# Optimization experiments

Hardware: AMD Instinct MI355X
Metric: run time of the kernel (lower is better)

Reference implementation:

```python
import jax, jax.numpy as jnp
import numpy as np

N = 1500                 # number of proposals
NUM_CLASSES = 81         # COCO: background + 80
NMS_THRESH = 0.5
SCORE_THRESH = 0.05
MAX_DET = 100            # config.test.max_det
BBOX_REG_WEIGHTS = jnp.array([10.0, 10.0, 5.0, 5.0], dtype=jnp.float32)


def setup_inputs() -> dict:
    key = jax.random.key(0)
    k1, k2, k3 = jax.random.split(key, 3)
    H, W = 800.0, 1333.0
    # realistic proposals: random centers / sizes inside the image
    cx = jax.random.uniform(jax.random.fold_in(k1, 0), (N,)) * W
    cy = jax.random.uniform(jax.random.fold_in(k1, 1), (N,)) * H
    bw = jax.random.uniform(jax.random.fold_in(k1, 2), (N,)) * 200.0 + 16.0
    bh = jax.random.uniform(jax.random.fold_in(k1, 3), (N,)) * 200.0 + 16.0
    bottom_rois = jnp.stack(
        [jnp.zeros((N,)), cx - 0.5 * bw, cy - 0.5 * bh, cx + 0.5 * bw, cy + 0.5 * bh],
        axis=1).astype(jnp.float32)
    bbox_delta = (jax.random.normal(k2, (N, 4 * NUM_CLASSES)) * 0.5).astype(jnp.float32)
    cls_prob = jax.nn.softmax(jax.random.normal(k3, (N, NUM_CLASSES)) * 2.0, axis=-1).astype(jnp.float32)
    im_info = jnp.array([[H, W, 1.0]], dtype=jnp.float32)
    return {"bottom_rois": bottom_rois, "bbox_delta": bbox_delta,
            "cls_prob": cls_prob, "im_info": im_info}


def _decode_boxes(rois, deltas, im_info):
    # rois [N,4], deltas [N,4C] -> clipped boxes [N,C,4] (legacy +1 convention)
    x1, y1, x2, y2 = rois[:, 0], rois[:, 1], rois[:, 2], rois[:, 3]
    w = x2 - x1 + 1.0
    h = y2 - y1 + 1.0
    cx = x1 + 0.5 * w
    cy = y1 + 0.5 * h
    d = deltas.reshape(deltas.shape[0], -1, 4) / BBOX_REG_WEIGHTS  # [N,C,4]
    pcx = cx[:, None] + w[:, None] * d[..., 0]
    pcy = cy[:, None] + h[:, None] * d[..., 1]
    pw = w[:, None] * jnp.exp(d[..., 2])
    ph = h[:, None] * jnp.exp(d[..., 3])
    boxes = jnp.stack([pcx - 0.5 * pw, pcy - 0.5 * ph,
                       pcx + 0.5 * pw - 1.0, pcy + 0.5 * ph - 1.0], axis=-1)
    hw = im_info[0, :2]  # [height, width]
    lim = jnp.stack([hw[1] - 1.0, hw[0] - 1.0, hw[1] - 1.0, hw[0] - 1.0])
    return jnp.clip(boxes, 0.0, lim)


def _pairwise_iou(b):
    # b [N,4], legacy +1 areas (matches gpu_nms)
    x1, y1, x2, y2 = b[:, 0], b[:, 1], b[:, 2], b[:, 3]
    area = (x2 - x1 + 1.0) * (y2 - y1 + 1.0)
    iw = jnp.maximum(jnp.minimum(x2[:, None], x2[None, :]) - jnp.maximum(x1[:, None], x1[None, :]) + 1.0, 0.0)
    ih = jnp.maximum(jnp.minimum(y2[:, None], y2[None, :]) - jnp.maximum(y1[:, None], y1[None, :]) + 1.0, 0.0)
    inter = iw * ih
    return inter / (area[:, None] + area[None, :] - inter)


def _nms_one_class(boxes, scores):
    # boxes [N,4], scores [N] -> score-sorted boxes/scores + keep mask
    valid = scores > SCORE_THRESH
    order = jnp.argsort(-scores)
    b = boxes[order]
    s = scores[order]
    v = valid[order]
    iou = jax.lax.stop_gradient(_pairwise_iou(b))  # used only in comparisons

    def body(suppressed, i):
        keep_i = v[i] & ~suppressed[i]
        suppressed = suppressed | (keep_i & (iou[i] > NMS_THRESH))
        return suppressed, keep_i

    _, keep = jax.lax.scan(body, jnp.zeros((b.shape[0],), bool), jnp.arange(b.shape[0]))
    return b, s, keep


def reference(bottom_rois, bbox_delta, cls_prob, im_info):
    boxes = _decode_boxes(bottom_rois[:, 1:], bbox_delta, im_info)  # [N,C,4]
    C = cls_prob.shape[1]
    boxes_fg = jnp.swapaxes(boxes, 0, 1)[1:]   # [C-1,N,4]
    scores_fg = cls_prob.T[1:]                 # [C-1,N]
    b, s, keep = jax.vmap(_nms_one_class)(boxes_fg, scores_fg)
    # image-level max_det cap (>= kth score, as in source)
    flat = jnp.where(keep, s, -jnp.inf).reshape(-1)
    n_keep = keep.sum()
    kth = jax.lax.top_k(flat, MAX_DET)[0][-1]
    keep = keep & jnp.where(n_keep > MAX_DET, s >= kth, True)
    cls_idx = jnp.broadcast_to(jnp.arange(1, C)[:, None], s.shape)
    zeros = jnp.zeros_like(s[..., None])
    dets = jnp.concatenate([zeros, b, s[..., None]], axis=-1)  # [C-1,N,6]
    dets = jnp.where(keep[..., None], dets, 0.0).reshape(-1, 6)
    return dets, cls_idx.reshape(-1), keep.reshape(-1)
```

## Files before the change

### kernel.cpp

```cpp
#include <hip/hip_runtime.h>
#include <math.h>

#pragma clang fp contract(off)

#define N_ROIS     1500
#define NUM_CLS    81
#define FG         80
#define MAXC       1536
#define NMS_T      0.5f
#define SCORE_T    0.05f
#define MAX_DET    100
#define TOTAL      (FG * N_ROIS)
#define TPB        256
#define K1_BLOCKS  256
#define K2_TPB     1024
#define NCHUNK     ((N_ROIS + TPB - 1) / TPB)
#define SUBCAP     8192

__device__ __forceinline__ unsigned f2s(float f) {
    unsigned u = __float_as_uint(f);
    return (u & 0x80000000u) ? ~u : (u | 0x80000000u);
}
__device__ __forceinline__ float s2f(unsigned u) {
    return __uint_as_float((u & 0x80000000u) ? (u & 0x7FFFFFFFu) : ~u);
}

__global__ __launch_bounds__(TPB) void nms_k1(
    const float* __restrict__ rois,
    const float* __restrict__ deltas,
    const float* __restrict__ prob,
    const float* __restrict__ iminfo,
    float4* __restrict__ keptBox,
    int*    __restrict__ keptRow,
    float*  __restrict__ keptScore,
    int*    __restrict__ ctrs,
    float*  __restrict__ out)
{
    const int tid  = threadIdx.x;
    const int lane = tid & 63;
    const int wv   = tid >> 6;
    const int b    = blockIdx.x;

    if (b >= FG) {
        const float4 z4 = make_float4(0.f, 0.f, 0.f, 0.f);
        const int stride = (K1_BLOCKS - FG) * TPB;
        int g = (b - FG) * TPB + tid;

        float4* dets4 = (float4*)out;
        for (int i = g; i < TOTAL * 6 / 4; i += stride) dets4[i] = z4;

        float4* cls4  = (float4*)(out + (size_t)TOTAL * 6);
        float4* keep4 = (float4*)(out + (size_t)TOTAL * 7);
        for (int i = g; i < TOTAL / 4; i += stride) {
            float fc = (float)((i * 4) / N_ROIS + 1);
            cls4[i]  = make_float4(fc, fc, fc, fc);
            keep4[i] = z4;
        }
        return;
    }

    __shared__ unsigned long long key[MAXC];
    __shared__ unsigned long long skey[MAXC];
    __shared__ float4 box4[MAXC];
    __shared__ float  areaA[MAXC];
    __shared__ unsigned char keepf[MAXC], supp[MAXC];
    __shared__ int mcnt;

    const int c = b + 1;
    const int cbase = b * N_ROIS;

    if (tid == 0) mcnt = 0;
    __syncthreads();

    float sv[NCHUNK];
    #pragma unroll
    for (int t = 0; t < NCHUNK; ++t) {
        int i = t * TPB + tid;
        sv[t] = (i < N_ROIS) ? prob[i * NUM_CLS + c] : 0.0f;
    }
    #pragma unroll
    for (int t = 0; t < NCHUNK; ++t) {
        int i = t * TPB + tid;
        bool val = (i < N_ROIS) && (sv[t] > SCORE_T);
        unsigned long long m = __ballot(val);
        int base = 0;
        if (lane == 0 && m) base = atomicAdd(&mcnt, __popcll(m));
        base = __shfl(base, 0, 64);
        if (val) {
            int pos = base + __popcll(m & ((1ull << lane) - 1ull));
            key[pos] = ((unsigned long long)(~f2s(sv[t])) << 32) | (unsigned)i;
        }
    }
    __syncthreads();
    const int M = mcnt;
    if (M == 0) return;

    for (int i = tid; i < M; i += TPB) {
        unsigned long long kk = key[i];
        int cnt = 0;
        #pragma unroll 4
        for (int j = 0; j < M; ++j) cnt += (int)(key[j] < kk);
        skey[cnt] = kk;
    }
    __syncthreads();

    const float Hm1 = iminfo[0] - 1.0f;
    const float Wm1 = iminfo[1] - 1.0f;
    for (int k = tid; k < M; k += TPB) {
        unsigned long long kk = skey[k];
        int i = (int)(kk & 0xFFFFFFFFu);
        const float* rp = rois + i * 5;
        float x1 = rp[1], y1 = rp[2], x2 = rp[3], y2 = rp[4];
        float w  = x2 - x1 + 1.0f;
        float h  = y2 - y1 + 1.0f;
        float cx = x1 + 0.5f * w;
        float cy = y1 + 0.5f * h;
        const float* dp = deltas + i * (4 * NUM_CLS) + c * 4;
        float dx = dp[0] / 10.0f, dy = dp[1] / 10.0f;
        float dw = dp[2] / 5.0f,  dh = dp[3] / 5.0f;
        float pcx = cx + w * dx;
        float pcy = cy + h * dy;
        float pw  = w * expf(dw);
        float ph  = h * expf(dh);
        float a1 = pcx - 0.5f * pw;
        float a2 = pcy - 0.5f * ph;
        float a3 = pcx + 0.5f * pw - 1.0f;
        float a4 = pcy + 0.5f * ph - 1.0f;
        a1 = fminf(fmaxf(a1, 0.0f), Wm1);
        a2 = fminf(fmaxf(a2, 0.0f), Hm1);
        a3 = fminf(fmaxf(a3, 0.0f), Wm1);
        a4 = fminf(fmaxf(a4, 0.0f), Hm1);
        box4[k]  = make_float4(a1, a2, a3, a4);
        areaA[k] = (a3 - a1 + 1.0f) * (a4 - a2 + 1.0f);
        keepf[k] = 0; supp[k] = 0;
    }
    __syncthreads();

    const int MW = (M + 63) >> 6;
    const bool fast = (M * MW <= MAXC);

    if (fast) {
        for (int r = wv; r < M; r += TPB / 64) {
            float4 br = box4[r];
            float  ar = areaA[r];
            const int w0 = r >> 6;
            if (lane == 0)
                for (int w = 0; w < w0; ++w) key[r * MW + w] = 0ull;
            for (int w = w0; w < MW; ++w) {
                int col = (w << 6) | lane;
                bool inb = (col < M);
                int j = inb ? col : 0;
                float4 bj = box4[j];
                float  aj = areaA[j];
                float iw = fminf(br.z, bj.z) - fmaxf(br.x, bj.x) + 1.0f;
                float ih = fminf(br.w, bj.w) - fmaxf(br.y, bj.y) + 1.0f;
                iw = fmaxf(iw, 0.0f);
                ih = fmaxf(ih, 0.0f);
                float inter = iw * ih;
                float iou = inter / ((ar + aj) - inter);
                bool pred = inb && (col > r) && (iou > NMS_T);
                unsigned long long mk = __ballot(pred);
                if (lane == 0) key[r * MW + w] = mk;
            }
        }
        __syncthreads();

        if (tid < 64) {
            const int lw = (tid < MW) ? tid : 0;
            unsigned long long acc = 0;
            unsigned long long mcur = key[lw];
            for (int k = 0; k < M; ++k) {
                unsigned long long mnext =
                    (k + 1 < M) ? key[(k + 1) * MW + lw] : 0ull;
                int bit = (int)((acc >> (k & 63)) & 1ull);
                int sup = __shfl(bit, k >> 6, 64);
                if (!sup) {
                    acc |= mcur;
                    if (tid == 0) keepf[k] = 1;
                }
                mcur = mnext;
            }
        }
        __syncthreads();
    } else {
        for (int k = 0; k < M; ++k) {
            if (!supp[k]) {
                if (tid == 0) keepf[k] = 1;
                float4 bk = box4[k];
                float  ak = areaA[k];
                for (int j = k + 1 + tid; j < M; j += TPB) {
                    float4 bj = box4[j];
                    float  aj = areaA[j];
                    float iw = fminf(bk.z, bj.z) - fmaxf(bk.x, bj.x) + 1.0f;
                    float ih = fminf(bk.w, bj.w) - fmaxf(bk.y, bj.y) + 1.0f;
                    iw = fmaxf(iw, 0.0f);
                    ih = fmaxf(ih, 0.0f);
                    float inter = iw * ih;
                    float iou = inter / ((ak + aj) - inter);
                    if (iou > NMS_T) supp[j] = 1;
                }
            }
            __syncthreads();
        }
    }

    for (int k = tid; k < M; k += TPB) {
        if (keepf[k]) {
            int p = atomicAdd(&ctrs[0], 1);
            keptRow[p]   = cbase + k;
            keptBox[p]   = box4[k];
            keptScore[p] = s2f(~(unsigned)(skey[k] >> 32));
        }
    }
}

__global__ __launch_bounds__(K2_TPB) void kth_patch_k2(
    const int*    __restrict__ ctrs,
    const int*    __restrict__ keptRow,
    const float4* __restrict__ keptBox,
    const float*  __restrict__ keptScore,
    float* __restrict__ out)
{
    __shared__ int hist4[4][256];
    __shared__ unsigned sub[SUBCAP];
    __shared__ int wtot[4];
    __shared__ unsigned s_d0, s_sp;
    __shared__ int s_kk, s_cnt;
    __shared__ float s_kth;

    const int tid  = threadIdx.x;
    const int lane = tid & 63;
    const int wv   = tid >> 6;
    const int hp   = wv & 3;
    const int n = ctrs[0];

    if (n > MAX_DET) {
        if (tid < 1024) {
            #pragma unroll
            for (int w = 0; w < 4; ++w) if (tid < 256) hist4[w][tid] = 0;
        }
        __syncthreads();
        for (int i = tid; i < n; i += K2_TPB)
            atomicAdd(&hist4[hp][f2s(keptScore[i]) >> 24], 1);
        __syncthreads();
        if (tid < 256) {
            const int h = hist4[0][tid] + hist4[1][tid] +
                          hist4[2][tid] + hist4[3][tid];
            int r = h;
            #pragma unroll
            for (int off = 1; off < 64; off <<= 1) {
                int o = __shfl_down(r, off, 64);
                if (lane + off < 64) r += o;
            }
            if (lane == 0) wtot[wv] = r;
        }
        __syncthreads();
        if (tid < 256) {
            const int h = hist4[0][tid] + hist4[1][tid] +
                          hist4[2][tid] + hist4[3][tid];
            int r = h;
            #pragma unroll
            for (int off = 1; off < 64; off <<= 1) {
                int o = __shfl_down(r, off, 64);
                if (lane + off < 64) r += o;
            }
            int hi = 0;
            #pragma unroll
            for (int w2 = 0; w2 < 4; ++w2) if (w2 > wv) hi += wtot[w2];
            const int S_ge = r + hi, S_gt = S_ge - h;
            if (S_gt < MAX_DET && S_ge >= MAX_DET) {
                s_d0 = (unsigned)tid;
                s_kk = MAX_DET - S_gt;
            }
        }
        if (tid == 0) { s_cnt = 0; s_sp = 0u; }
        __syncthreads();
        const unsigned d0 = s_d0;

        for (int i0 = 0; i0 < n; i0 += K2_TPB) {
            int i = i0 + tid;
            unsigned u = (i < n) ? f2s(keptScore[i]) : 0u;
            bool match = (i < n) && ((u >> 24) == d0);
            unsigned long long m = __ballot(match);
            int base = 0;
            if (lane == 0 && m) base = atomicAdd(&s_cnt, __popcll(m));
            base = __shfl(base, 0, 64);
            if (match) {
                int pos = base + __popcll(m & ((1ull << lane) - 1ull));
                if (pos < SUBCAP) sub[pos] = u & 0xFFFFFFu;
            }
        }
        __syncthreads();
        const int ns = s_cnt;
        const bool inLds = (ns <= SUBCAP);
        const int limit = inLds ? ns : n;

        for (int d = 1; d < 4; ++d) {
            const int shift = 24 - 8 * d;
            if (tid < 256) {
                #pragma unroll
                for (int w = 0; w < 4; ++w) hist4[w][tid] = 0;
            }
            __syncthreads();
            const unsigned sp = s_sp;
            for (int i = tid; i < limit; i += K2_TPB) {
                unsigned v; bool ok;
                if (inLds) { v = sub[i]; ok = true; }
                else {
                    unsigned u = f2s(keptScore[i]);
                    ok = ((u >> 24) == d0);
                    v = u & 0xFFFFFFu;
                }
                if (ok && (d == 1 || (v >> (shift + 8)) == sp))
                    atomicAdd(&hist4[hp][(v >> shift) & 255u], 1);
            }
            __syncthreads();
            if (tid < 256) {
                const int h = hist4[0][tid] + hist4[1][tid] +
                              hist4[2][tid] + hist4[3][tid];
                int r = h;
                #pragma unroll
                for (int off = 1; off < 64; off <<= 1) {
                    int o = __shfl_down(r, off, 64);
                    if (lane + off < 64) r += o;
                }
                if (lane == 0) wtot[wv] = r;
            }
            __syncthreads();
            if (tid < 256) {
                const int h = hist4[0][tid] + hist4[1][tid] +
                              hist4[2][tid] + hist4[3][tid];
                int r = h;
                #pragma unroll
                for (int off = 1; off < 64; off <<= 1) {
                    int o = __shfl_down(r, off, 64);
                    if (lane + off < 64) r += o;
                }
                int hi = 0;
                #pragma unroll
                for (int w2 = 0; w2 < 4; ++w2) if (w2 > wv) hi += wtot[w2];
                const int S_ge = r + hi, S_gt = S_ge - h;
                const int kk = s_kk;
                if (S_gt < kk && S_ge >= kk) {
                    s_sp = (s_sp << 8) | (unsigned)tid;
                    s_kk = kk - S_gt;
                }
            }
            __syncthreads();
        }
        if (tid == 0) s_kth = s2f((s_d0 << 24) | s_sp);
    } else {
        if (tid == 0) s_kth = -INFINITY;
    }
    __syncthreads();
    const float kth = s_kth;

    for (int i = tid; i < n; i += K2_TPB) {
        float s = keptScore[i];
        if (s >= kth) {
            int r = keptRow[i];
            float4 b4 = keptBox[i];
            float* dst = out + (size_t)r * 6;
            dst[1] = b4.x; dst[2] = b4.y; dst[3] = b4.z; dst[4] = b4.w; dst[5] = s;
            out[(size_t)TOTAL * 7 + r] = 1.0f;
        }
    }
}

extern "C" void kernel_launch(void* const* d_in, const int* in_sizes, int n_in,
                              void* d_out, int out_size, void* d_ws, size_t ws_size,
                              hipStream_t stream) {
    const float* rois   = (const float*)d_in[0];
    const float* deltas = (const float*)d_in[1];
    const float* prob   = (const float*)d_in[2];
    const float* iminfo = (const float*)d_in[3];
    float* out = (float*)d_out;

    float4* keptBox   = (float4*)d_ws;
    int*    keptRow   = (int*)(keptBox + TOTAL);
    float*  keptScore = (float*)(keptRow + TOTAL);
    int*    ctrs      = (int*)(keptScore + TOTAL);

    hipMemsetAsync(ctrs, 0, sizeof(int), stream);
    nms_k1<<<K1_BLOCKS, TPB, 0, stream>>>(rois, deltas, prob, iminfo,
                                          keptBox, keptRow, keptScore, ctrs, out);
    kth_patch_k2<<<1, K2_TPB, 0, stream>>>(ctrs, keptRow, keptBox, keptScore, out);
}
```

Before: 105.0 us.

## Pack kept detections into per-class key segments and recompute boxes in patch kernel

Kept detections are now written as 64-bit keys (score, roi index, rank) into per-class workspace segments with per-class counts, replacing the global atomic counter, the box/row/score arrays and the memset launch. The second kernel radix-selects the kth score directly on these keys and re-decodes boxes from the raw inputs for survivors. In the first kernel, rank sorting is merged with box decoding, and each thread's own ROI and delta loads are issued before the sort to hide load latency. The aim is less global traffic and contention, plus one fewer launch, paid for by recomputing decode in the serial single-block kernel.

```diff
diff --git a/kernel.cpp b/kernel.cpp
--- a/kernel.cpp
+++ b/kernel.cpp
@@ -16,6 +16,7 @@
 #define K2_TPB     1024
 #define NCHUNK     ((N_ROIS + TPB - 1) / TPB)
 #define SUBCAP     8192
+#define SEG        N_ROIS
 
 __device__ __forceinline__ unsigned f2s(float f) {
     unsigned u = __float_as_uint(f);
@@ -23,6 +24,33 @@
 }
 __device__ __forceinline__ float s2f(unsigned u) {
     return __uint_as_float((u & 0x80000000u) ? (u & 0x7FFFFFFFu) : ~u);
+}
+
+__device__ __forceinline__ float4 decode_box(
+    float x1, float y1, float x2, float y2,
+    float dx0, float dy0, float dw0, float dh0,
+    float Hm1, float Wm1, float* area)
+{
+    float w  = x2 - x1 + 1.0f;
+    float h  = y2 - y1 + 1.0f;
+    float cx = x1 + 0.5f * w;
+    float cy = y1 + 0.5f * h;
+    float dx = dx0 / 10.0f, dy = dy0 / 10.0f;
+    float dw = dw0 / 5.0f,  dh = dh0 / 5.0f;
+    float pcx = cx + w * dx;
+    float pcy = cy + h * dy;
+    float pw  = w * expf(dw);
+    float ph  = h * expf(dh);
+    float a1 = pcx - 0.5f * pw;
+    float a2 = pcy - 0.5f * ph;
+    float a3 = pcx + 0.5f * pw - 1.0f;
+    float a4 = pcy + 0.5f * ph - 1.0f;
+    a1 = fminf(fmaxf(a1, 0.0f), Wm1);
+    a2 = fminf(fmaxf(a2, 0.0f), Hm1);
+    a3 = fminf(fmaxf(a3, 0.0f), Wm1);
+    a4 = fminf(fmaxf(a4, 0.0f), Hm1);
+    *area = (a3 - a1 + 1.0f) * (a4 - a2 + 1.0f);
+    return make_float4(a1, a2, a3, a4);
 }
 
 __global__ __launch_bounds__(TPB) void nms_k1(
@@ -30,11 +58,9 @@
     const float* __restrict__ deltas,
     const float* __restrict__ prob,
     const float* __restrict__ iminfo,
-    float4* __restrict__ keptBox,
-    int*    __restrict__ keptRow,
-    float*  __restrict__ keptScore,
-    int*    __restrict__ ctrs,
-    float*  __restrict__ out)
+    unsigned long long* __restrict__ keptKey,
+    int* __restrict__ cnt,
+    float* __restrict__ out)
 {
     const int tid  = threadIdx.x;
     const int lane = tid & 63;
@@ -64,12 +90,11 @@
     __shared__ float4 box4[MAXC];
     __shared__ float  areaA[MAXC];
     __shared__ unsigned char keepf[MAXC], supp[MAXC];
-    __shared__ int mcnt;
+    __shared__ int mcnt, lcnt;
 
     const int c = b + 1;
-    const int cbase = b * N_ROIS;
-
-    if (tid == 0) mcnt = 0;
+
+    if (tid == 0) { mcnt = 0; lcnt = 0; }
     __syncthreads();
 
     float sv[NCHUNK];
@@ -93,46 +118,47 @@
     }
     __syncthreads();
     const int M = mcnt;
-    if (M == 0) return;
-
-    for (int i = tid; i < M; i += TPB) {
-        unsigned long long kk = key[i];
-        int cnt = 0;
-        #pragma unroll 4
-        for (int j = 0; j < M; ++j) cnt += (int)(key[j] < kk);
-        skey[cnt] = kk;
-    }
-    __syncthreads();
+    if (M == 0) { if (tid == 0) cnt[b] = 0; return; }
 
     const float Hm1 = iminfo[0] - 1.0f;
     const float Wm1 = iminfo[1] - 1.0f;
-    for (int k = tid; k < M; k += TPB) {
-        unsigned long long kk = skey[k];
+
+    const bool own = (tid < M);
+    float x1 = 0.f, y1 = 0.f, x2 = 0.f, y2 = 0.f;
+    float d0 = 0.f, d1 = 0.f, d2 = 0.f, d3 = 0.f;
+    int myrank = 0;
+    if (own) {
+        unsigned long long kk = key[tid];
         int i = (int)(kk & 0xFFFFFFFFu);
         const float* rp = rois + i * 5;
-        float x1 = rp[1], y1 = rp[2], x2 = rp[3], y2 = rp[4];
-        float w  = x2 - x1 + 1.0f;
-        float h  = y2 - y1 + 1.0f;
-        float cx = x1 + 0.5f * w;
-        float cy = y1 + 0.5f * h;
+        x1 = rp[1]; y1 = rp[2]; x2 = rp[3]; y2 = rp[4];
         const float* dp = deltas + i * (4 * NUM_CLS) + c * 4;
-        float dx = dp[0] / 10.0f, dy = dp[1] / 10.0f;
-        float dw = dp[2] / 5.0f,  dh = dp[3] / 5.0f;
-        float pcx = cx + w * dx;
-        float pcy = cy + h * dy;
-        float pw  = w * expf(dw);
-        float ph  = h * expf(dh);
-        float a1 = pcx - 0.5f * pw;
-        float a2 = pcy - 0.5f * ph;
-        float a3 = pcx + 0.5f * pw - 1.0f;
-        float a4 = pcy + 0.5f * ph - 1.0f;
-        a1 = fminf(fmaxf(a1, 0.0f), Wm1);
-        a2 = fminf(fmaxf(a2, 0.0f), Hm1);
-        a3 = fminf(fmaxf(a3, 0.0f), Wm1);
-        a4 = fminf(fmaxf(a4, 0.0f), Hm1);
-        box4[k]  = make_float4(a1, a2, a3, a4);
-        areaA[k] = (a3 - a1 + 1.0f) * (a4 - a2 + 1.0f);
-        keepf[k] = 0; supp[k] = 0;
+        d0 = dp[0]; d1 = dp[1]; d2 = dp[2]; d3 = dp[3];
+    }
+
+    for (int ii = tid; ii < M; ii += TPB) {
+        unsigned long long kk = key[ii];
+        int cr = 0;
+        #pragma unroll 4
+        for (int j = 0; j < M; ++j) cr += (int)(key[j] < kk);
+        skey[cr] = kk;
+        keepf[ii] = 0; supp[ii] = 0;
+        if (ii == tid) {
+            myrank = cr;
+        } else {
+            int i = (int)(kk & 0xFFFFFFFFu);
+            const float* rp = rois + i * 5;
+            const float* dp = deltas + i * (4 * NUM_CLS) + c * 4;
+            float ar;
+            float4 bx = decode_box(rp[1], rp[2], rp[3], rp[4],
+                                   dp[0], dp[1], dp[2], dp[3], Hm1, Wm1, &ar);
+            box4[cr] = bx; areaA[cr] = ar;
+        }
+    }
+    if (own) {
+        float ar;
+        float4 bx = decode_box(x1, y1, x2, y2, d0, d1, d2, d3, Hm1, Wm1, &ar);
+        box4[myrank] = bx; areaA[myrank] = ar;
     }
     __syncthreads();
 
@@ -204,165 +230,167 @@
         }
     }
 
+    const int seg = b * SEG;
     for (int k = tid; k < M; k += TPB) {
         if (keepf[k]) {
-            int p = atomicAdd(&ctrs[0], 1);
-            keptRow[p]   = cbase + k;
-            keptBox[p]   = box4[k];
-            keptScore[p] = s2f(~(unsigned)(skey[k] >> 32));
+            int p = atomicAdd(&lcnt, 1);
+            unsigned long long sk = skey[k];
+            unsigned u = ~(unsigned)(sk >> 32);
+            keptKey[seg + p] = ((unsigned long long)u << 32) |
+                               ((sk & 0xFFFFull) << 16) |
+                               (unsigned long long)(unsigned)k;
+        }
+    }
+    __syncthreads();
+    if (tid == 0) cnt[b] = lcnt;
+}
+
+__device__ __forceinline__ void digit_pick(
+    int (*h4)[256], int* wtot, unsigned* s_sp, int* s_kk,
+    int tid, int lane, int wv)
+{
+    int h = 0, r = 0, kk = 0;
+    if (tid < 256) {
+        h = h4[0][tid] + h4[1][tid] + h4[2][tid] + h4[3][tid];
+        r = h;
+        #pragma unroll
+        for (int off = 1; off < 64; off <<= 1) {
+            int o = __shfl_down(r, off, 64);
+            if (lane + off < 64) r += o;
+        }
+        if (lane == 0) wtot[wv] = r;
+        kk = *s_kk;
+    }
+    __syncthreads();
+    if (tid < 256) {
+        int hi = 0;
+        #pragma unroll
+        for (int w2 = 0; w2 < 4; ++w2) if (w2 > wv) hi += wtot[w2];
+        const int S_ge = r + hi, S_gt = S_ge - h;
+        if (S_gt < kk && S_ge >= kk) {
+            *s_sp = (*s_sp << 8) | (unsigned)tid;
+            *s_kk = kk - S_gt;
         }
     }
 }
 
 __global__ __launch_bounds__(K2_TPB) void kth_patch_k2(
-    const int*    __restrict__ ctrs,
-    const int*    __restrict__ keptRow,
-    const float4* __restrict__ keptBox,
-    const float*  __restrict__ keptScore,
+    const int* __restrict__ cnt,
+    const unsigned long long* __restrict__ keptKey,
+    const float* __restrict__ rois,
+    const float* __restrict__ deltas,
+    const float* __restrict__ iminfo,
     float* __restrict__ out)
 {
+    __shared__ int scnt[FG];
     __shared__ int hist4[4][256];
     __shared__ unsigned sub[SUBCAP];
     __shared__ int wtot[4];
-    __shared__ unsigned s_d0, s_sp;
-    __shared__ int s_kk, s_cnt;
-    __shared__ float s_kth;
+    __shared__ int s_n, s_pos, s_kk;
+    __shared__ unsigned s_sp;
 
     const int tid  = threadIdx.x;
     const int lane = tid & 63;
     const int wv   = tid >> 6;
     const int hp   = wv & 3;
-    const int n = ctrs[0];
+
+    if (tid < FG) scnt[tid] = cnt[tid];
+    if (tid == 0) { s_pos = 0; s_sp = 0u; s_kk = MAX_DET; }
+    __syncthreads();
+    if (tid == 0) {
+        int t = 0;
+        for (int s = 0; s < FG; ++s) t += scnt[s];
+        s_n = t;
+    }
+    __syncthreads();
+    const int n = s_n;
 
     if (n > MAX_DET) {
-        if (tid < 1024) {
-            #pragma unroll
-            for (int w = 0; w < 4; ++w) if (tid < 256) hist4[w][tid] = 0;
-        }
-        __syncthreads();
-        for (int i = tid; i < n; i += K2_TPB)
-            atomicAdd(&hist4[hp][f2s(keptScore[i]) >> 24], 1);
-        __syncthreads();
-        if (tid < 256) {
-            const int h = hist4[0][tid] + hist4[1][tid] +
-                          hist4[2][tid] + hist4[3][tid];
-            int r = h;
-            #pragma unroll
-            for (int off = 1; off < 64; off <<= 1) {
-                int o = __shfl_down(r, off, 64);
-                if (lane + off < 64) r += o;
-            }
-            if (lane == 0) wtot[wv] = r;
-        }
-        __syncthreads();
-        if (tid < 256) {
-            const int h = hist4[0][tid] + hist4[1][tid] +
-                          hist4[2][tid] + hist4[3][tid];
-            int r = h;
-            #pragma unroll
-            for (int off = 1; off < 64; off <<= 1) {
-                int o = __shfl_down(r, off, 64);
-                if (lane + off < 64) r += o;
-            }
-            int hi = 0;
-            #pragma unroll
-            for (int w2 = 0; w2 < 4; ++w2) if (w2 > wv) hi += wtot[w2];
-            const int S_ge = r + hi, S_gt = S_ge - h;
-            if (S_gt < MAX_DET && S_ge >= MAX_DET) {
-                s_d0 = (unsigned)tid;
-                s_kk = MAX_DET - S_gt;
-            }
-        }
-        if (tid == 0) { s_cnt = 0; s_sp = 0u; }
-        __syncthreads();
-        const unsigned d0 = s_d0;
-
-        for (int i0 = 0; i0 < n; i0 += K2_TPB) {
-            int i = i0 + tid;
-            unsigned u = (i < n) ? f2s(keptScore[i]) : 0u;
-            bool match = (i < n) && ((u >> 24) == d0);
-            unsigned long long m = __ballot(match);
-            int base = 0;
-            if (lane == 0 && m) base = atomicAdd(&s_cnt, __popcll(m));
-            base = __shfl(base, 0, 64);
-            if (match) {
-                int pos = base + __popcll(m & ((1ull << lane) - 1ull));
-                if (pos < SUBCAP) sub[pos] = u & 0xFFFFFFu;
-            }
-        }
-        __syncthreads();
-        const int ns = s_cnt;
-        const bool inLds = (ns <= SUBCAP);
-        const int limit = inLds ? ns : n;
-
-        for (int d = 1; d < 4; ++d) {
-            const int shift = 24 - 8 * d;
-            if (tid < 256) {
-                #pragma unroll
-                for (int w = 0; w < 4; ++w) hist4[w][tid] = 0;
+        const bool inLds = (n <= SUBCAP);
+        if (inLds) {
+            for (int s = wv; s < FG; s += K2_TPB / 64) {
+                const int c = scnt[s];
+                const unsigned long long* kp = keptKey + s * SEG;
+                for (int i0 = 0; i0 < c; i0 += 64) {
+                    int i = i0 + lane;
+                    bool ok = (i < c);
+                    unsigned u = ok ? (unsigned)(kp[i] >> 32) : 0u;
+                    int cc = c - i0; if (cc > 64) cc = 64;
+                    int basep = 0;
+                    if (lane == 0) basep = atomicAdd(&s_pos, cc);
+                    basep = __shfl(basep, 0, 64);
+                    if (ok) sub[basep + lane] = u;
+                }
             }
             __syncthreads();
-            const unsigned sp = s_sp;
-            for (int i = tid; i < limit; i += K2_TPB) {
-                unsigned v; bool ok;
-                if (inLds) { v = sub[i]; ok = true; }
-                else {
-                    unsigned u = f2s(keptScore[i]);
-                    ok = ((u >> 24) == d0);
-                    v = u & 0xFFFFFFu;
-                }
-                if (ok && (d == 1 || (v >> (shift + 8)) == sp))
-                    atomicAdd(&hist4[hp][(v >> shift) & 255u], 1);
-            }
-            __syncthreads();
-            if (tid < 256) {
-                const int h = hist4[0][tid] + hist4[1][tid] +
-                              hist4[2][tid] + hist4[3][tid];
-                int r = h;
-                #pragma unroll
-                for (int off = 1; off < 64; off <<= 1) {
-                    int o = __shfl_down(r, off, 64);
-                    if (lane + off < 64) r += o;
-                }
-                if (lane == 0) wtot[wv] = r;
-            }
-            __syncthreads();
-            if (tid < 256) {
-                const int h = hist4[0][tid] + hist4[1][tid] +
-                              hist4[2][tid] + hist4[3][tid];
-                int r = h;
-                #pragma unroll
-                for (int off = 1; off < 64; off <<= 1) {
-                    int o = __shfl_down(r, off, 64);
-                    if (lane + off < 64) r += o;
-                }
-                int hi = 0;
-                #pragma unroll
-                for (int w2 = 0; w2 < 4; ++w2) if (w2 > wv) hi += wtot[w2];
-                const int S_ge = r + hi, S_gt = S_ge - h;
-                const int kk = s_kk;
-                if (S_gt < kk && S_ge >= kk) {
-                    s_sp = (s_sp << 8) | (unsigned)tid;
-                    s_kk = kk - S_gt;
-                }
-            }
-            __syncthreads();
-        }
-        if (tid == 0) s_kth = s2f((s_d0 << 24) | s_sp);
-    } else {
-        if (tid == 0) s_kth = -INFINITY;
-    }
-    __syncthreads();
-    const float kth = s_kth;
-
-    for (int i = tid; i < n; i += K2_TPB) {
-        float s = keptScore[i];
-        if (s >= kth) {
-            int r = keptRow[i];
-            float4 b4 = keptBox[i];
-            float* dst = out + (size_t)r * 6;
-            dst[1] = b4.x; dst[2] = b4.y; dst[3] = b4.z; dst[4] = b4.w; dst[5] = s;
-            out[(size_t)TOTAL * 7 + r] = 1.0f;
+            for (int d = 0; d < 4; ++d) {
+                const int shift = 24 - 8 * d;
+                if (tid < 256) {
+                    hist4[0][tid] = 0; hist4[1][tid] = 0;
+                    hist4[2][tid] = 0; hist4[3][tid] = 0;
+                }
+                __syncthreads();
+                const unsigned pre = s_sp;
+                for (int i = tid; i < n; i += K2_TPB) {
+                    unsigned v = sub[i];
+                    if (d == 0 || (v >> (shift + 8)) == pre)
+                        atomicAdd(&hist4[hp][(v >> shift) & 255u], 1);
+                }
+                __syncthreads();
+                digit_pick(hist4, wtot, &s_sp, &s_kk, tid, lane, wv);
+                __syncthreads();
+            }
+        } else {
+            for (int d = 0; d < 4; ++d) {
+                const int shift = 24 - 8 * d;
+                if (tid < 256) {
+                    hist4[0][tid] = 0; hist4[1][tid] = 0;
+                    hist4[2][tid] = 0; hist4[3][tid] = 0;
+                }
+                __syncthreads();
+                const unsigned pre = s_sp;
+                for (int s = wv; s < FG; s += K2_TPB / 64) {
+                    const int c = scnt[s];
+                    const unsigned long long* kp = keptKey + s * SEG;
+                    for (int i = lane; i < c; i += 64) {
+                        unsigned v = (unsigned)(kp[i] >> 32);
+                        if (d == 0 || (v >> (shift + 8)) == pre)
+                            atomicAdd(&hist4[hp][(v >> shift) & 255u], 1);
+                    }
+                }
+                __syncthreads();
+                digit_pick(hist4, wtot, &s_sp, &s_kk, tid, lane, wv);
+                __syncthreads();
+            }
+        }
+    }
+    __syncthreads();
+    const unsigned ukth = (n > MAX_DET) ? s_sp : 0u;
+
+    const float Hm1 = iminfo[0] - 1.0f;
+    const float Wm1 = iminfo[1] - 1.0f;
+
+    for (int s = wv; s < FG; s += K2_TPB / 64) {
+        const int c = scnt[s];
+        const unsigned long long* kp = keptKey + s * SEG;
+        for (int idx = lane; idx < c; idx += 64) {
+            unsigned long long key = kp[idx];
+            unsigned u = (unsigned)(key >> 32);
+            if (u >= ukth) {
+                int i = (int)((key >> 16) & 0xFFFFu);
+                int k = (int)(key & 0xFFFFu);
+                int r = s * N_ROIS + k;
+                const float* rp = rois + i * 5;
+                const float* dp = deltas + i * (4 * NUM_CLS) + (s + 1) * 4;
+                float ar;
+                float4 b4 = decode_box(rp[1], rp[2], rp[3], rp[4],
+                                       dp[0], dp[1], dp[2], dp[3],
+                                       Hm1, Wm1, &ar);
+                float* dst = out + (size_t)r * 6;
+                dst[1] = b4.x; dst[2] = b4.y; dst[3] = b4.z;
+                dst[4] = b4.w; dst[5] = s2f(u);
+                out[(size_t)TOTAL * 7 + r] = 1.0f;
+            }
         }
     }
 }
@@ -376,13 +404,11 @@
     const float* iminfo = (const float*)d_in[3];
     float* out = (float*)d_out;
 
-    float4* keptBox   = (float4*)d_ws;
-    int*    keptRow   = (int*)(keptBox + TOTAL);
-    float*  keptScore = (float*)(keptRow + TOTAL);
-    int*    ctrs      = (int*)(keptScore + TOTAL);
-
-    hipMemsetAsync(ctrs, 0, sizeof(int), stream);
+    unsigned long long* keptKey = (unsigned long long*)d_ws;
+    int* cnt = (int*)(keptKey + FG * SEG);
+
     nms_k1<<<K1_BLOCKS, TPB, 0, stream>>>(rois, deltas, prob, iminfo,
-                                          keptBox, keptRow, keptScore, ctrs, out);
-    kth_patch_k2<<<1, K2_TPB, 0, stream>>>(ctrs, keptRow, keptBox, keptScore, out);
-}
+                                          keptKey, cnt, out);
+    kth_patch_k2<<<1, K2_TPB, 0, stream>>>(cnt, keptKey, rois, deltas,
+                                           iminfo, out);
+}
```

Measured after the change: 107.4 us. +2.3%, slower.
